# Kernel tuning notes

Measured on AMD Instinct MI355X. Metric: run time of the kernel, lower is better.

The kernel has to match this reference:

```python
import jax, jax.numpy as jnp
import numpy as np
import math

RES = 320
DECIMATION = 4
M = RES * RES // DECIMATION  # 25600 trajectory points
OVERSAMP = 1.25
WIDTH = 4
BETA = math.pi * (((WIDTH / OVERSAMP) * (OVERSAMP - 0.5)) ** 2 - 0.8) ** 0.5
B = 16


def setup_inputs() -> dict:
    key = jax.random.key(0)
    k1, k2 = jax.random.split(key)
    k_space_input = jax.random.normal(k1, (B, 1, RES, RES, 2), dtype=jnp.float32)
    # learnable k-space trajectory, coords in [-RES/2, RES/2)
    trajectory = (jax.random.uniform(k2, (M, 2), dtype=jnp.float32) - 0.5) * RES
    return {"k_space_input": k_space_input, "trajectory": trajectory}


def _grid_sample_bilinear(img, traj):
    # img: [B, C, H, W]; traj: [M, 2] = (x, y) in [-res/2, res/2]
    # Matches torch grid_sample(align_corners=True, padding_mode='zeros')
    # after normalizing traj by (res/2).
    Bn, C, H, W = img.shape
    gx = traj[:, 0] / (W / 2)
    gy = traj[:, 1] / (H / 2)
    px = (gx + 1.0) * 0.5 * (W - 1)
    py = (gy + 1.0) * 0.5 * (H - 1)
    x0 = jnp.floor(px)
    y0 = jnp.floor(py)
    wx1 = px - x0
    wy1 = py - y0
    out = jnp.zeros((Bn, C, traj.shape[0]), img.dtype)
    for dy in (0, 1):
        for dx in (0, 1):
            xi = x0 + dx
            yi = y0 + dy
            w = (wx1 if dx else 1.0 - wx1) * (wy1 if dy else 1.0 - wy1)
            inb = (xi >= 0) & (xi < W) & (yi >= 0) & (yi < H)
            xc = jnp.clip(xi, 0, W - 1).astype(jnp.int32)
            yc = jnp.clip(yi, 0, H - 1).astype(jnp.int32)
            out = out + img[:, :, yc, xc] * (w * inb)[None, None, :]
    return out  # [B, C, M]


def _kb_weight(delta, half):
    # Kaiser-Bessel interpolation kernel (sigpy convention, 1/width factor per dim)
    x = delta / half
    t = jnp.maximum(1.0 - x * x, 0.0)
    return jnp.i0(BETA * jnp.sqrt(t)) / WIDTH


def _nufft_adjoint(y, coord, H, W):
    # y: [B, M] complex64; coord: [M,2], coord[:,0]->H axis, coord[:,1]->W axis
    osH = math.ceil(OVERSAMP * H)
    osW = math.ceil(OVERSAMP * W)
    scale = jnp.array([osH / H, osW / W], jnp.float32)
    shift = jnp.array([osH // 2, osW // 2], jnp.float32)
    c = coord * scale + shift  # scaled to oversampled-grid coords
    half = WIDTH / 2.0
    start = jnp.ceil(c - half)                       # [M,2]
    offs = jnp.arange(WIDTH, dtype=jnp.float32)
    idx = start[:, :, None] + offs                   # [M,2,WIDTH]
    w = _kb_weight(c[:, :, None] - idx, half)        # [M,2,WIDTH]
    iy = idx[:, 0].astype(jnp.int32) % osH           # [M,WIDTH]
    ix = idx[:, 1].astype(jnp.int32) % osW
    ww = w[:, 0, :, None] * w[:, 1, None, :]         # [M,WIDTH,WIDTH]
    flat = (iy[:, :, None] * osW + ix[:, None, :]).reshape(-1)  # [M*WIDTH^2]
    Bn = y.shape[0]
    contrib = (y[:, :, None, None] * ww[None]).reshape(Bn, -1)  # [B, M*WIDTH^2]
    grid = jnp.zeros((Bn, osH * osW), y.dtype).at[:, flat].add(contrib)
    grid = grid.reshape(Bn, osH, osW)
    # centered unnormalized-to-ortho IFFT (sigpy scaling)
    img = jnp.fft.fftshift(
        jnp.fft.ifft2(jnp.fft.ifftshift(grid, axes=(-2, -1)), axes=(-2, -1)),
        axes=(-2, -1))
    img = img * ((osH * osW) / math.sqrt(H * W))
    sy = osH // 2 - H // 2
    sx = osW // 2 - W // 2
    img = img[:, sy:sy + H, sx:sx + W]  # center crop

    def apod(n, os_n):
        a = jnp.sqrt(jnp.maximum(
            BETA ** 2 - (np.pi * WIDTH * (jnp.arange(n, dtype=jnp.float32) - n // 2) / os_n) ** 2,
            1e-12))
        return a / jnp.sinh(a)

    img = img * apod(H, osH)[:, None] * apod(W, osW)[None, :]
    return img  # [B, H, W] complex


def reference(k_space_input, trajectory):
    # [B,1,H,W,2] -> [B,2,H,W] (real/imag channels)
    ksp = jnp.transpose(k_space_input, (0, 1, 4, 2, 3))[:, 0]
    sub = _grid_sample_bilinear(ksp, trajectory)          # [B,2,M]
    y = (sub[:, 0] + 1j * sub[:, 1]).astype(jnp.complex64)
    img = _nufft_adjoint(y, trajectory, ksp.shape[-2], ksp.shape[-1])
    out = jnp.stack([img.real, img.imag], axis=1)          # [B,2,H,W]
    return out[:, None]                                    # [B,1,2,H,W]
```

## Files before the change

### kernel.cpp

```cpp
#include <hip/hip_runtime.h>
#include <hip/hip_fp16.h>

#define NPTS   25600
#define NB     16
#define NRES   320
#define OS     400
#define NCELL  (OS * OS)
#define CAP    16
#define MAXOVF 4096

#define NJA    8
#define NJB    5
#define FFTTH  512
#define LSTRV  404

#define BETA_F (3.14159265358979f * 2.22710574513201f)

struct H2X2 { __half2 a, b; };

__device__ __forceinline__ float bessel_i0f(float x) {
    float ax = fabsf(x);
    if (ax < 3.75f) {
        float t = (ax * ax) * (1.0f / 14.0625f);
        return 1.0f + t * (3.5156229f + t * (3.0899424f + t * (1.2067492f +
                     t * (0.2659732f + t * (0.0360768f + t * 0.0045813f)))));
    } else {
        float t = 3.75f / ax;
        return (expf(ax) * rsqrtf(ax)) *
               (0.39894228f + t * (0.01328592f + t * (0.00225319f + t * (-0.00157565f +
                t * (0.00916281f + t * (-0.02057706f + t * (0.02635537f +
                t * (-0.01647633f + t * 0.00392377f))))))));
    }
}

struct OvfEntry { int cell; int m; float w; float pad; };

__global__ __launch_bounds__(1024)
void k_transpose(const float2* __restrict__ ksp, float2* __restrict__ kspT,
                 int* __restrict__ cursor, int* __restrict__ ovf_cnt)
{
    __shared__ float2 T[8 * 8 * 17];
    int tid = threadIdx.x;
    int bx = blockIdx.x % 40, by = blockIdx.x / 40;
    int x0 = bx * 8, y0 = by * 8;

    int cbase = blockIdx.x * 100;
    if (tid < 100) cursor[cbase + tid] = 0;
    if (blockIdx.x == 0 && tid >= 100 && tid < 116) ovf_cnt[tid - 100] = 0;

    int b  = tid >> 6, yl = (tid >> 3) & 7, xl = tid & 7;
    T[(yl * 8 + xl) * 17 + b] = ksp[((size_t)b * NRES + (y0 + yl)) * NRES + x0 + xl];
    __syncthreads();

    int yl2 = tid >> 7, xl2 = (tid >> 4) & 7, b2 = tid & 15;
    kspT[((size_t)(y0 + yl2) * NRES + x0 + xl2) * NB + b2] = T[(yl2 * 8 + xl2) * 17 + b2];
}

__global__ __launch_bounds__(256)
void k_sample_taps(const float2* __restrict__ kspT,
                   const float* __restrict__ traj,
                   float2* __restrict__ val,
                   int* __restrict__ cursor,
                   float2* __restrict__ entries,
                   int* __restrict__ ovf_cnt,
                   OvfEntry* __restrict__ ovf)
{
    int blk = blockIdx.x;
    if (blk < 1600) {
        int gid = blk * 256 + threadIdx.x;
        int b = gid & 15;
        int m = gid >> 4;

        float tx = traj[2 * m + 0];
        float ty = traj[2 * m + 1];

        float px = (tx * (1.0f / 160.0f) + 1.0f) * 0.5f * 319.0f;
        float py = (ty * (1.0f / 160.0f) + 1.0f) * 0.5f * 319.0f;
        float fx0 = floorf(px), fy0 = floorf(py);
        int x0 = (int)fx0, y0 = (int)fy0;
        float wx1 = px - fx0, wy1 = py - fy0;
        float wx0 = 1.0f - wx1, wy0 = 1.0f - wy1;

        const float2* row0 = kspT + ((size_t)y0 * NRES + x0) * NB + b;
        const float2* row1 = row0 + (size_t)NRES * NB;
        float2 v00 = row0[0];
        float2 v01 = row0[NB];
        float2 v10 = row1[0];
        float2 v11 = row1[NB];
        float sr = (v00.x * wx0 + v01.x * wx1) * wy0 + (v10.x * wx0 + v11.x * wx1) * wy1;
        float si = (v00.y * wx0 + v01.y * wx1) * wy0 + (v10.y * wx0 + v11.y * wx1) * wy1;

        val[gid] = make_float2(sr, si);
    } else {
        int g = (blk - 1600) * 256 + threadIdx.x;
        int m = g >> 2;
        int tq = g & 3;
        if (m >= NPTS) return;

        float tx = traj[2 * m + 0];
        float ty = traj[2 * m + 1];
        float c0 = tx * 1.25f + 200.0f;
        float c1 = ty * 1.25f + 200.0f;
        float s0 = ceilf(c0 - 2.0f);
        float s1 = ceilf(c1 - 2.0f);

        float id0 = s0 + (float)tq;
        float d0 = (c0 - id0) * 0.5f;
        float t0v = fmaxf(1.0f - d0 * d0, 0.0f);
        float w0 = bessel_i0f(BETA_F * sqrtf(t0v)) * (0.25f / 320.0f);
        int   i0 = (((int)id0) + OS) % OS;

        float w1[4];
        int   i1[4];
#pragma unroll
        for (int t = 0; t < 4; t++) {
            float id1 = s1 + (float)t;
            float d1 = (c1 - id1) * 0.5f;
            float t1 = fmaxf(1.0f - d1 * d1, 0.0f);
            w1[t] = bessel_i0f(BETA_F * sqrtf(t1)) * 0.25f;
            i1[t] = (((int)id1) + OS) % OS;
        }

#pragma unroll
        for (int t1 = 0; t1 < 4; t1++) {
            int cell = i1[t1] * OS + i0;
            float w = w0 * w1[t1];
            int slot = atomicAdd(&cursor[cell], 1);
            if (slot < CAP) {
                entries[(size_t)slot * NCELL + cell] = make_float2(__int_as_float(m), w);
            } else {
                int oi = atomicAdd(ovf_cnt, 1);
                if (oi < MAXOVF) { ovf[oi].cell = cell; ovf[oi].m = m; ovf[oi].w = w; }
            }
        }
    }
}

__global__ __launch_bounds__(256)
void k_gather(const int* __restrict__ cursor,
              const float2* __restrict__ entries,
              const float4* __restrict__ val4,
              __half2* __restrict__ grid,
              const int* __restrict__ ovf_cnt,
              const OvfEntry* __restrict__ ovf)
{
    int t = threadIdx.x;
    int half = t >> 7;
    int cell = blockIdx.x * 128 + (t & 127);
    if (cell >= NCELL) return;
    int cnt_raw = cursor[cell];
    int cnt = min(cnt_raw, CAP);

    float4 acc[4];
#pragma unroll
    for (int q = 0; q < 4; q++) acc[q] = make_float4(0.f, 0.f, 0.f, 0.f);

    for (int k = 0; k < cnt; k++) {
        float2 e = entries[(size_t)k * NCELL + cell];
        int m = __float_as_int(e.x);
        float w = e.y;
        const float4* v = val4 + (size_t)m * 8 + half * 4;
#pragma unroll
        for (int q = 0; q < 4; q++) {
            float4 x = v[q];
            acc[q].x = fmaf(w, x.x, acc[q].x);
            acc[q].y = fmaf(w, x.y, acc[q].y);
            acc[q].z = fmaf(w, x.z, acc[q].z);
            acc[q].w = fmaf(w, x.w, acc[q].w);
        }
    }

    if (cnt_raw > CAP) {
        int n = min(*ovf_cnt, MAXOVF);
        for (int i = 0; i < n; i++) {
            if (ovf[i].cell != cell) continue;
            int m = ovf[i].m;
            float w = ovf[i].w;
            const float4* v = val4 + (size_t)m * 8 + half * 4;
#pragma unroll
            for (int q = 0; q < 4; q++) {
                float4 x = v[q];
                acc[q].x = fmaf(w, x.x, acc[q].x);
                acc[q].y = fmaf(w, x.y, acc[q].y);
                acc[q].z = fmaf(w, x.z, acc[q].z);
                acc[q].w = fmaf(w, x.w, acc[q].w);
            }
        }
    }

#pragma unroll
    for (int q = 0; q < 4; q++) {
        int p = half * 8 + 2 * q;
        grid[(size_t)(p + 0) * NCELL + cell] = __float22half2_rn(make_float2(acc[q].x, acc[q].y));
        grid[(size_t)(p + 1) * NCELL + cell] = __float22half2_rn(make_float2(acc[q].z, acc[q].w));
    }
}

__device__ __forceinline__ void dft20_conj(const float2* __restrict__ Al, int off, int kh,
                                           const float2* __restrict__ E20t,
                                           float& y1r, float& y1i, float& y2r, float& y2i)
{
    float2 x0 = Al[off], x10 = Al[off + 200];
    if (kh == 0) {
        float br = x0.x + x10.x, bi = x0.y + x10.y;
        float ar = 0.f, ai = 0.f, dr = 0.f, di = 0.f;
#pragma unroll
        for (int j = 1; j <= 9; j++) {
            float2 xa = Al[off + 20 * j];
            float2 xb = Al[off + 400 - 20 * j];
            float pr = xa.x + xb.x, pi = xa.y + xb.y;
            ar += pr; ai += pi;
            float sg = (j & 1) ? -1.f : 1.f;
            dr = fmaf(sg, pr, dr); di = fmaf(sg, pi, di);
        }
        y1r = br + ar; y1i = bi + ai;
        y2r = br + dr; y2i = bi + di;
    } else {
        float sgn = (kh & 1) ? -1.f : 1.f;
        float br = fmaf(sgn, x10.x, x0.x), bi = fmaf(sgn, x10.y, x0.y);
        float2 ek = E20t[kh];
        float c = ek.x, s = ek.y;
        float Asr = 0.f, Asi = 0.f, Bsr = 0.f, Bsi = 0.f;
#pragma unroll
        for (int j = 1; j <= 9; j++) {
            float2 xa = Al[off + 20 * j];
            float2 xb = Al[off + 400 - 20 * j];
            float pr = xa.x + xb.x, pi = xa.y + xb.y;
            float mr = xa.x - xb.x, mi = xa.y - xb.y;
            Asr = fmaf(c, pr, Asr); Asi = fmaf(c, pi, Asi);
            Bsr = fmaf(s, mi, Bsr); Bsi = fmaf(s, mr, Bsi);
            float cn = c * ek.x - s * ek.y;
            s = c * ek.y + s * ek.x;
            c = cn;
        }
        y1r = br + Asr - Bsr; y1i = bi + Asi + Bsi;
        y2r = br + Asr + Bsr; y2i = bi + Asi - Bsi;
    }
}

__device__ __forceinline__ float apodf(int i) {
    float t = (float)(i - 160) * 0.031415926535897932f;
    float a = sqrtf(fmaxf(BETA_F * BETA_F - t * t, 1e-12f));
    return a / sinhf(a);
}

__global__ __launch_bounds__(FFTTH, 4)
void k_fft_pass_a(const __half2* __restrict__ grid, __half2* __restrict__ At)
{
    __shared__ __align__(16) float2 A[NJA * LSTRV];
    __shared__ float2 E20t[20];
    __shared__ float2 E400p[424];
    int tid = threadIdx.x;
    int b = blockIdx.y;
    int j0 = blockIdx.x * NJA;

    if (tid < 400) {
        float sn, cs;
        sincosf((float)tid * 0.015707963267948966f, &sn, &cs);
        E400p[tid + (tid >> 4)] = make_float2(cs, sn);
    } else if (tid >= 448 && tid < 468) {
        int t = tid - 448;
        float sn, cs;
        sincosf((float)t * 0.3141592653589793f, &sn, &cs);
        E20t[t] = make_float2(cs, sn);
    }

    const H2X2* g2 = (const H2X2*)(grid + (size_t)b * NCELL + (size_t)j0 * OS);
    for (int o = tid; o < NJA * 200; o += FFTTH) {
        int r = o / 200, q = o - r * 200;
        H2X2 v = g2[o];
        A[r * LSTRV + 2 * q]     = __half22float2(v.a);
        A[r * LSTRV + 2 * q + 1] = __half22float2(v.b);
    }
    __syncthreads();

    float v1r[4], v1i[4], v2r[4], v2i[4];
#pragma unroll
    for (int it = 0; it < 4; it++) {
        int o = tid + it * FFTTH;
        if (o < NJA * 200) {
            int r = o / 200, q = o - r * 200;
            int kh = q / 20, n2 = q - kh * 20;
            float y1r, y1i, y2r, y2i;
            dft20_conj(&A[r * LSTRV], n2, kh, E20t, y1r, y1i, y2r, y2i);
            if (kh == 0) {
                v1r[it] = y1r; v1i[it] = y1i;
                int ti = 10 * n2;
                float2 tw = E400p[ti + (ti >> 4)];
                v2r[it] = y2r * tw.x - y2i * tw.y; v2i[it] = y2r * tw.y + y2i * tw.x;
            } else {
                int t1 = n2 * kh, t2 = n2 * (20 - kh);
                float2 w1 = E400p[t1 + (t1 >> 4)], w2 = E400p[t2 + (t2 >> 4)];
                v1r[it] = y1r * w1.x - y1i * w1.y; v1i[it] = y1r * w1.y + y1i * w1.x;
                v2r[it] = y2r * w2.x - y2i * w2.y; v2i[it] = y2r * w2.y + y2i * w2.x;
            }
        }
    }
    __syncthreads();
#pragma unroll
    for (int it = 0; it < 4; it++) {
        int o = tid + it * FFTTH;
        if (o < NJA * 200) {
            int r = o / 200, q = o - r * 200;
            int kh = q / 20, n2 = q - kh * 20;
            float2* Al = &A[r * LSTRV + 20 * n2];
            if (kh == 0) {
                Al[0]  = make_float2(v1r[it], v1i[it]);
                Al[10] = make_float2(v2r[it], v2i[it]);
            } else {
                Al[kh]      = make_float2(v1r[it], v1i[it]);
                Al[20 - kh] = make_float2(v2r[it], v2i[it]);
            }
        }
    }
    __syncthreads();

#pragma unroll
    for (int it = 0; it < 3; it++) {
        int o = tid + it * FFTTH;
        if (o < NJA * 180) {
            int r = o / 180, q = o - r * 180;
            int k2h = q / 20, k1 = q - k2h * 20;
            float y1r, y1i, y2r, y2i;
            dft20_conj(&A[r * LSTRV], k1, k2h, E20t, y1r, y1i, y2r, y2i);
            v1r[it] = y1r; v1i[it] = y1i;
            v2r[it] = y2r; v2i[it] = y2i;
        }
    }
    __syncthreads();
#pragma unroll
    for (int it = 0; it < 3; it++) {
        int o = tid + it * FFTTH;
        if (o < NJA * 180) {
            int r = o / 180, q = o - r * 180;
            int k2h = q / 20, k1 = q - k2h * 20;
            float2* Al = &A[r * LSTRV];
            if (k2h == 0) {
                Al[k1] = make_float2(v1r[it], v1i[it]);
            } else {
                if (k2h <= 7)
                    Al[20 * k2h + k1] = make_float2(v1r[it], v1i[it]);
                Al[320 - 20 * k2h + k1] = make_float2(v2r[it], v2i[it]);
            }
        }
    }
    __syncthreads();

    for (int o = tid; o < 320 * NJA; o += FFTTH) {
        int uc = o >> 3, r = o & 7;
        At[((size_t)b * 320 + uc) * OS + j0 + r] = __float22half2_rn(A[r * LSTRV + uc]);
    }
}

__global__ __launch_bounds__(FFTTH, 4)
void k_fft_pass_b(const __half2* __restrict__ At, float* __restrict__ out)
{
    __shared__ __align__(16) float2 A[NJB * LSTRV];
    __shared__ float2 E20t[20];
    __shared__ float2 E400p[424];
    __shared__ float apodT[320];
    int tid = threadIdx.x;
    int b = blockIdx.y;
    int uc0 = blockIdx.x * NJB;

    if (tid < 400) {
        float sn, cs;
        sincosf((float)tid * 0.015707963267948966f, &sn, &cs);
        E400p[tid + (tid >> 4)] = make_float2(cs, sn);
    } else if (tid >= 448 && tid < 468) {
        int t = tid - 448;
        float sn, cs;
        sincosf((float)t * 0.3141592653589793f, &sn, &cs);
        E20t[t] = make_float2(cs, sn);
    }
    if (tid < 320) apodT[tid] = apodf(tid);

    const H2X2* a2 = (const H2X2*)(At + ((size_t)b * 320 + uc0) * OS);
    for (int o = tid; o < NJB * 200; o += FFTTH) {
        int r = o / 200, q = o - r * 200;
        H2X2 v = a2[o];
        A[r * LSTRV + 2 * q]     = __half22float2(v.a);
        A[r * LSTRV + 2 * q + 1] = __half22float2(v.b);
    }
    __syncthreads();

    float v1r[2], v1i[2], v2r[2], v2i[2];
#pragma unroll
    for (int it = 0; it < 2; it++) {
        int o = tid + it * FFTTH;
        if (o < NJB * 200) {
            int r = o / 200, q = o - r * 200;
            int kh = q / 20, n2 = q - kh * 20;
            float y1r, y1i, y2r, y2i;
            dft20_conj(&A[r * LSTRV], n2, kh, E20t, y1r, y1i, y2r, y2i);
            if (kh == 0) {
                v1r[it] = y1r; v1i[it] = y1i;
                int ti = 10 * n2;
                float2 tw = E400p[ti + (ti >> 4)];
                v2r[it] = y2r * tw.x - y2i * tw.y; v2i[it] = y2r * tw.y + y2i * tw.x;
            } else {
                int t1 = n2 * kh, t2 = n2 * (20 - kh);
                float2 w1 = E400p[t1 + (t1 >> 4)], w2 = E400p[t2 + (t2 >> 4)];
                v1r[it] = y1r * w1.x - y1i * w1.y; v1i[it] = y1r * w1.y + y1i * w1.x;
                v2r[it] = y2r * w2.x - y2i * w2.y; v2i[it] = y2r * w2.y + y2i * w2.x;
            }
        }
    }
    __syncthreads();
#pragma unroll
    for (int it = 0; it < 2; it++) {
        int o = tid + it * FFTTH;
        if (o < NJB * 200) {
            int r = o / 200, q = o - r * 200;
            int kh = q / 20, n2 = q - kh * 20;
            float2* Al = &A[r * LSTRV + 20 * n2];
            if (kh == 0) {
                Al[0]  = make_float2(v1r[it], v1i[it]);
                Al[10] = make_float2(v2r[it], v2i[it]);
            } else {
                Al[kh]      = make_float2(v1r[it], v1i[it]);
                Al[20 - kh] = make_float2(v2r[it], v2i[it]);
            }
        }
    }
    __syncthreads();

    for (int o = tid; o < NJB * 180; o += FFTTH) {
        int r = o / 180, q = o - r * 180;
        int k2h = q / 20, k1 = q - k2h * 20;
        float y1r, y1i, y2r, y2i;
        dft20_conj(&A[r * LSTRV], k1, k2h, E20t, y1r, y1i, y2r, y2i);

        int y = uc0 + r + 160; if (y >= 320) y -= 320;
        float apy = apodT[y];
        float* o0 = out + (((size_t)b * 2 + 0) * NRES + y) * NRES;
        float* o1 = out + (((size_t)b * 2 + 1) * NRES + y) * NRES;

        if (k2h <= 7) {
            int vc = 20 * k2h + k1;
            int x = vc + 160; if (x >= 320) x -= 320;
            float sg = ((x + y) & 1) ? -1.0f : 1.0f;
            float sc = sg * apy * apodT[x];
            o0[x] = y1r * sc;
            o1[x] = y1i * sc;
        }
        if (k2h >= 1) {
            int vc = 320 - 20 * k2h + k1;
            int x = vc + 160; if (x >= 320) x -= 320;
            float sg = ((x + y) & 1) ? -1.0f : 1.0f;
            float sc = sg * apy * apodT[x];
            o0[x] = y2r * sc;
            o1[x] = y2i * sc;
        }
    }
}

extern "C" void kernel_launch(void* const* d_in, const int* in_sizes, int n_in,
                              void* d_out, int out_size, void* d_ws, size_t ws_size,
                              hipStream_t stream) {
    const float* ksp  = (const float*)d_in[0];
    const float* traj = (const float*)d_in[1];
    float* out = (float*)d_out;

    float* base = (float*)d_ws;
    __half2* grid_h = (__half2*)base;
    __half2* At_h   = (__half2*)(base + (size_t)NB * NCELL);
    float2* entries = (float2*)(base + (size_t)NB * NCELL + (size_t)NB * 320 * OS);
    float2* val  = entries + (size_t)CAP * NCELL;
    float2* kspT = val + (size_t)NPTS * NB;
    int* cursor  = (int*)(kspT + (size_t)NRES * NRES * NB);
    int* ovf_cnt = cursor + NCELL;
    OvfEntry* ovf = (OvfEntry*)(ovf_cnt + 16);

    k_transpose  <<<dim3(1600), 1024, 0, stream>>>((const float2*)ksp, kspT, cursor, ovf_cnt);
    k_sample_taps<<<dim3(2000), 256, 0, stream>>>(kspT, traj, val, cursor, entries, ovf_cnt, ovf);
    k_gather     <<<dim3(NCELL / 128), 256, 0, stream>>>(cursor, entries, (const float4*)val,
                                                         grid_h, ovf_cnt, ovf);
    k_fft_pass_a <<<dim3(OS / NJA, NB),  FFTTH, 0, stream>>>(grid_h, At_h);
    k_fft_pass_b <<<dim3(320 / NJB, NB), FFTTH, 0, stream>>>(At_h, out);
}
```

Measured before the change: 131.0 us.

## Fuse cell gather into first FFT pass and spread taps over threads

Removes the separate gather kernel and the half-precision oversampled grid buffer. The first FFT pass now builds each row in shared memory directly from the per-cell entry lists and the sampled values, accumulating in fp32. This saves one launch plus a full grid write and read-back. The tap-binning kernel also moves from 4 threads per point to 16, one thread per 2D tap, to expose more parallelism. In exchange, every batch block re-reads the cell entry lists and does scattered 8-byte value loads, which is 16x redundant index traffic compared with the old gather that served all batches at once.

Measured after the change: 173.3 us. 1.32x slower.

```diff
diff --git a/kernel.cpp b/kernel.cpp
--- a/kernel.cpp
+++ b/kernel.cpp
@@ -93,106 +93,38 @@
         val[gid] = make_float2(sr, si);
     } else {
         int g = (blk - 1600) * 256 + threadIdx.x;
-        int m = g >> 2;
-        int tq = g & 3;
-        if (m >= NPTS) return;
+        int m   = g >> 4;
+        int tap = g & 15;
+        int t0  = tap & 3, t1 = tap >> 2;
 
         float tx = traj[2 * m + 0];
         float ty = traj[2 * m + 1];
         float c0 = tx * 1.25f + 200.0f;
         float c1 = ty * 1.25f + 200.0f;
-        float s0 = ceilf(c0 - 2.0f);
-        float s1 = ceilf(c1 - 2.0f);
-
-        float id0 = s0 + (float)tq;
+        float s0f = ceilf(c0 - 2.0f);
+        float s1f = ceilf(c1 - 2.0f);
+
+        float id0 = s0f + (float)t0;
         float d0 = (c0 - id0) * 0.5f;
         float t0v = fmaxf(1.0f - d0 * d0, 0.0f);
         float w0 = bessel_i0f(BETA_F * sqrtf(t0v)) * (0.25f / 320.0f);
         int   i0 = (((int)id0) + OS) % OS;
 
-        float w1[4];
-        int   i1[4];
-#pragma unroll
-        for (int t = 0; t < 4; t++) {
-            float id1 = s1 + (float)t;
-            float d1 = (c1 - id1) * 0.5f;
-            float t1 = fmaxf(1.0f - d1 * d1, 0.0f);
-            w1[t] = bessel_i0f(BETA_F * sqrtf(t1)) * 0.25f;
-            i1[t] = (((int)id1) + OS) % OS;
-        }
-
-#pragma unroll
-        for (int t1 = 0; t1 < 4; t1++) {
-            int cell = i1[t1] * OS + i0;
-            float w = w0 * w1[t1];
-            int slot = atomicAdd(&cursor[cell], 1);
-            if (slot < CAP) {
-                entries[(size_t)slot * NCELL + cell] = make_float2(__int_as_float(m), w);
-            } else {
-                int oi = atomicAdd(ovf_cnt, 1);
-                if (oi < MAXOVF) { ovf[oi].cell = cell; ovf[oi].m = m; ovf[oi].w = w; }
-            }
-        }
-    }
-}
-
-__global__ __launch_bounds__(256)
-void k_gather(const int* __restrict__ cursor,
-              const float2* __restrict__ entries,
-              const float4* __restrict__ val4,
-              __half2* __restrict__ grid,
-              const int* __restrict__ ovf_cnt,
-              const OvfEntry* __restrict__ ovf)
-{
-    int t = threadIdx.x;
-    int half = t >> 7;
-    int cell = blockIdx.x * 128 + (t & 127);
-    if (cell >= NCELL) return;
-    int cnt_raw = cursor[cell];
-    int cnt = min(cnt_raw, CAP);
-
-    float4 acc[4];
-#pragma unroll
-    for (int q = 0; q < 4; q++) acc[q] = make_float4(0.f, 0.f, 0.f, 0.f);
-
-    for (int k = 0; k < cnt; k++) {
-        float2 e = entries[(size_t)k * NCELL + cell];
-        int m = __float_as_int(e.x);
-        float w = e.y;
-        const float4* v = val4 + (size_t)m * 8 + half * 4;
-#pragma unroll
-        for (int q = 0; q < 4; q++) {
-            float4 x = v[q];
-            acc[q].x = fmaf(w, x.x, acc[q].x);
-            acc[q].y = fmaf(w, x.y, acc[q].y);
-            acc[q].z = fmaf(w, x.z, acc[q].z);
-            acc[q].w = fmaf(w, x.w, acc[q].w);
-        }
-    }
-
-    if (cnt_raw > CAP) {
-        int n = min(*ovf_cnt, MAXOVF);
-        for (int i = 0; i < n; i++) {
-            if (ovf[i].cell != cell) continue;
-            int m = ovf[i].m;
-            float w = ovf[i].w;
-            const float4* v = val4 + (size_t)m * 8 + half * 4;
-#pragma unroll
-            for (int q = 0; q < 4; q++) {
-                float4 x = v[q];
-                acc[q].x = fmaf(w, x.x, acc[q].x);
-                acc[q].y = fmaf(w, x.y, acc[q].y);
-                acc[q].z = fmaf(w, x.z, acc[q].z);
-                acc[q].w = fmaf(w, x.w, acc[q].w);
-            }
-        }
-    }
-
-#pragma unroll
-    for (int q = 0; q < 4; q++) {
-        int p = half * 8 + 2 * q;
-        grid[(size_t)(p + 0) * NCELL + cell] = __float22half2_rn(make_float2(acc[q].x, acc[q].y));
-        grid[(size_t)(p + 1) * NCELL + cell] = __float22half2_rn(make_float2(acc[q].z, acc[q].w));
+        float id1 = s1f + (float)t1;
+        float d1 = (c1 - id1) * 0.5f;
+        float t1v = fmaxf(1.0f - d1 * d1, 0.0f);
+        float w1 = bessel_i0f(BETA_F * sqrtf(t1v)) * 0.25f;
+        int   i1 = (((int)id1) + OS) % OS;
+
+        int cell = i1 * OS + i0;
+        float w = w0 * w1;
+        int slot = atomicAdd(&cursor[cell], 1);
+        if (slot < CAP) {
+            entries[(size_t)slot * NCELL + cell] = make_float2(__int_as_float(m), w);
+        } else {
+            int oi = atomicAdd(ovf_cnt, 1);
+            if (oi < MAXOVF) { ovf[oi].cell = cell; ovf[oi].m = m; ovf[oi].w = w; }
+        }
     }
 }
 
@@ -245,7 +177,12 @@
 }
 
 __global__ __launch_bounds__(FFTTH, 4)
-void k_fft_pass_a(const __half2* __restrict__ grid, __half2* __restrict__ At)
+void k_fft_pass_a(const int* __restrict__ cursor,
+                  const float2* __restrict__ entries,
+                  const float2* __restrict__ val,
+                  const int* __restrict__ ovf_cnt,
+                  const OvfEntry* __restrict__ ovf,
+                  __half2* __restrict__ At)
 {
     __shared__ __align__(16) float2 A[NJA * LSTRV];
     __shared__ float2 E20t[20];
@@ -265,12 +202,30 @@
         E20t[t] = make_float2(cs, sn);
     }
 
-    const H2X2* g2 = (const H2X2*)(grid + (size_t)b * NCELL + (size_t)j0 * OS);
-    for (int o = tid; o < NJA * 200; o += FFTTH) {
-        int r = o / 200, q = o - r * 200;
-        H2X2 v = g2[o];
-        A[r * LSTRV + 2 * q]     = __half22float2(v.a);
-        A[r * LSTRV + 2 * q + 1] = __half22float2(v.b);
+    for (int o = tid; o < NJA * OS; o += FFTTH) {
+        int r = o / OS, x = o - r * OS;
+        int cell = (j0 + r) * OS + x;
+        int cnt_raw = cursor[cell];
+        int cnt = min(cnt_raw, CAP);
+        float ar = 0.f, ai = 0.f;
+        for (int k = 0; k < cnt; k++) {
+            float2 e = entries[(size_t)k * NCELL + cell];
+            int mm = __float_as_int(e.x);
+            float w = e.y;
+            float2 v = val[(size_t)mm * NB + b];
+            ar = fmaf(w, v.x, ar);
+            ai = fmaf(w, v.y, ai);
+        }
+        if (cnt_raw > CAP) {
+            int n = min(*ovf_cnt, MAXOVF);
+            for (int i = 0; i < n; i++) {
+                if (ovf[i].cell != cell) continue;
+                float2 v = val[(size_t)ovf[i].m * NB + b];
+                ar = fmaf(ovf[i].w, v.x, ar);
+                ai = fmaf(ovf[i].w, v.y, ai);
+            }
+        }
+        A[r * LSTRV + x] = make_float2(ar, ai);
     }
     __syncthreads();
 
@@ -463,9 +418,8 @@
     float* out = (float*)d_out;
 
     float* base = (float*)d_ws;
-    __half2* grid_h = (__half2*)base;
-    __half2* At_h   = (__half2*)(base + (size_t)NB * NCELL);
-    float2* entries = (float2*)(base + (size_t)NB * NCELL + (size_t)NB * 320 * OS);
+    __half2* At_h   = (__half2*)base;
+    float2* entries = (float2*)(base + (size_t)NB * 320 * OS);
     float2* val  = entries + (size_t)CAP * NCELL;
     float2* kspT = val + (size_t)NPTS * NB;
     int* cursor  = (int*)(kspT + (size_t)NRES * NRES * NB);
@@ -473,9 +427,7 @@
     OvfEntry* ovf = (OvfEntry*)(ovf_cnt + 16);
 
     k_transpose  <<<dim3(1600), 1024, 0, stream>>>((const float2*)ksp, kspT, cursor, ovf_cnt);
-    k_sample_taps<<<dim3(2000), 256, 0, stream>>>(kspT, traj, val, cursor, entries, ovf_cnt, ovf);
-    k_gather     <<<dim3(NCELL / 128), 256, 0, stream>>>(cursor, entries, (const float4*)val,
-                                                         grid_h, ovf_cnt, ovf);
-    k_fft_pass_a <<<dim3(OS / NJA, NB),  FFTTH, 0, stream>>>(grid_h, At_h);
+    k_sample_taps<<<dim3(3200), 256, 0, stream>>>(kspT, traj, val, cursor, entries, ovf_cnt, ovf);
+    k_fft_pass_a <<<dim3(OS / NJA, NB),  FFTTH, 0, stream>>>(cursor, entries, val, ovf_cnt, ovf, At_h);
     k_fft_pass_b <<<dim3(320 / NJB, NB), FFTTH, 0, stream>>>(At_h, out);
 }
```

## Fuse sampling, tap binning and gather into one cooperative kernel with grid sync

Applied to the files above, without the earlier changes.

Merges the bilinear sampling/tap-binning kernel and the per-cell gather kernel into one cooperative kernel. The two phases are separated by a grid-wide barrier and use grid-stride loops over 1024 blocks of 256 threads. Tap work is also remapped so each thread computes one of the 16 taps rather than four, which spreads the Bessel evaluations and atomics across more lanes. This removes one kernel launch boundary, but adds grid-sync cost and requires all 1024 blocks to be co-resident.

After: 238.9 us. 1.82x slower.

```diff
diff --git a/kernel.cpp b/kernel.cpp
--- a/kernel.cpp
+++ b/kernel.cpp
@@ -1,5 +1,8 @@
 #include <hip/hip_runtime.h>
 #include <hip/hip_fp16.h>
+#include <hip/hip_cooperative_groups.h>
+
+namespace cg = cooperative_groups;
 
 #define NPTS   25600
 #define NB     16
@@ -13,6 +16,10 @@
 #define NJB    5
 #define FFTTH  512
 #define LSTRV  404
+
+#define MIDBLK 1024
+#define MIDTH  256
+#define MIDN   (MIDBLK * MIDTH)
 
 #define BETA_F (3.14159265358979f * 2.22710574513201f)
 
@@ -56,75 +63,66 @@
     kspT[((size_t)(y0 + yl2) * NRES + x0 + xl2) * NB + b2] = T[(yl2 * 8 + xl2) * 17 + b2];
 }
 
-__global__ __launch_bounds__(256)
-void k_sample_taps(const float2* __restrict__ kspT,
-                   const float* __restrict__ traj,
-                   float2* __restrict__ val,
-                   int* __restrict__ cursor,
-                   float2* __restrict__ entries,
-                   int* __restrict__ ovf_cnt,
-                   OvfEntry* __restrict__ ovf)
+__global__ __launch_bounds__(MIDTH, 4)
+void k_mid(const float2* __restrict__ kspT,
+           const float* __restrict__ traj,
+           float2* __restrict__ val,
+           int* __restrict__ cursor,
+           float2* __restrict__ entries,
+           int* __restrict__ ovf_cnt,
+           OvfEntry* __restrict__ ovf,
+           __half2* __restrict__ grid)
 {
-    int blk = blockIdx.x;
-    if (blk < 1600) {
-        int gid = blk * 256 + threadIdx.x;
-        int b = gid & 15;
-        int m = gid >> 4;
-
+    cg::grid_group gg = cg::this_grid();
+    int gtid = blockIdx.x * MIDTH + threadIdx.x;
+
+    for (int i = gtid; i < NPTS * NB; i += MIDN) {
+        int m = i >> 4;
         float tx = traj[2 * m + 0];
         float ty = traj[2 * m + 1];
 
-        float px = (tx * (1.0f / 160.0f) + 1.0f) * 0.5f * 319.0f;
-        float py = (ty * (1.0f / 160.0f) + 1.0f) * 0.5f * 319.0f;
-        float fx0 = floorf(px), fy0 = floorf(py);
-        int x0 = (int)fx0, y0 = (int)fy0;
-        float wx1 = px - fx0, wy1 = py - fy0;
-        float wx0 = 1.0f - wx1, wy0 = 1.0f - wy1;
-
-        const float2* row0 = kspT + ((size_t)y0 * NRES + x0) * NB + b;
-        const float2* row1 = row0 + (size_t)NRES * NB;
-        float2 v00 = row0[0];
-        float2 v01 = row0[NB];
-        float2 v10 = row1[0];
-        float2 v11 = row1[NB];
-        float sr = (v00.x * wx0 + v01.x * wx1) * wy0 + (v10.x * wx0 + v11.x * wx1) * wy1;
-        float si = (v00.y * wx0 + v01.y * wx1) * wy0 + (v10.y * wx0 + v11.y * wx1) * wy1;
-
-        val[gid] = make_float2(sr, si);
-    } else {
-        int g = (blk - 1600) * 256 + threadIdx.x;
-        int m = g >> 2;
-        int tq = g & 3;
-        if (m >= NPTS) return;
-
-        float tx = traj[2 * m + 0];
-        float ty = traj[2 * m + 1];
-        float c0 = tx * 1.25f + 200.0f;
-        float c1 = ty * 1.25f + 200.0f;
-        float s0 = ceilf(c0 - 2.0f);
-        float s1 = ceilf(c1 - 2.0f);
-
-        float id0 = s0 + (float)tq;
-        float d0 = (c0 - id0) * 0.5f;
-        float t0v = fmaxf(1.0f - d0 * d0, 0.0f);
-        float w0 = bessel_i0f(BETA_F * sqrtf(t0v)) * (0.25f / 320.0f);
-        int   i0 = (((int)id0) + OS) % OS;
-
-        float w1[4];
-        int   i1[4];
-#pragma unroll
-        for (int t = 0; t < 4; t++) {
-            float id1 = s1 + (float)t;
+        {
+            int b = i & 15;
+            float px = (tx * (1.0f / 160.0f) + 1.0f) * 0.5f * 319.0f;
+            float py = (ty * (1.0f / 160.0f) + 1.0f) * 0.5f * 319.0f;
+            float fx0 = floorf(px), fy0 = floorf(py);
+            int x0 = (int)fx0, y0 = (int)fy0;
+            float wx1 = px - fx0, wy1 = py - fy0;
+            float wx0 = 1.0f - wx1, wy0 = 1.0f - wy1;
+
+            const float2* row0 = kspT + ((size_t)y0 * NRES + x0) * NB + b;
+            const float2* row1 = row0 + (size_t)NRES * NB;
+            float2 v00 = row0[0];
+            float2 v01 = row0[NB];
+            float2 v10 = row1[0];
+            float2 v11 = row1[NB];
+            float sr = (v00.x * wx0 + v01.x * wx1) * wy0 + (v10.x * wx0 + v11.x * wx1) * wy1;
+            float si = (v00.y * wx0 + v01.y * wx1) * wy0 + (v10.y * wx0 + v11.y * wx1) * wy1;
+            val[i] = make_float2(sr, si);
+        }
+
+        {
+            int tap = i & 15;
+            int t0 = tap & 3, t1 = tap >> 2;
+            float c0 = tx * 1.25f + 200.0f;
+            float c1 = ty * 1.25f + 200.0f;
+            float s0f = ceilf(c0 - 2.0f);
+            float s1f = ceilf(c1 - 2.0f);
+
+            float id0 = s0f + (float)t0;
+            float d0 = (c0 - id0) * 0.5f;
+            float t0v = fmaxf(1.0f - d0 * d0, 0.0f);
+            float w0 = bessel_i0f(BETA_F * sqrtf(t0v)) * (0.25f / 320.0f);
+            int   i0 = (((int)id0) + OS) % OS;
+
+            float id1 = s1f + (float)t1;
             float d1 = (c1 - id1) * 0.5f;
-            float t1 = fmaxf(1.0f - d1 * d1, 0.0f);
-            w1[t] = bessel_i0f(BETA_F * sqrtf(t1)) * 0.25f;
-            i1[t] = (((int)id1) + OS) % OS;
-        }
-
-#pragma unroll
-        for (int t1 = 0; t1 < 4; t1++) {
-            int cell = i1[t1] * OS + i0;
-            float w = w0 * w1[t1];
+            float t1v = fmaxf(1.0f - d1 * d1, 0.0f);
+            float w1 = bessel_i0f(BETA_F * sqrtf(t1v)) * 0.25f;
+            int   i1 = (((int)id1) + OS) % OS;
+
+            int cell = i1 * OS + i0;
+            float w = w0 * w1;
             int slot = atomicAdd(&cursor[cell], 1);
             if (slot < CAP) {
                 entries[(size_t)slot * NCELL + cell] = make_float2(__int_as_float(m), w);
@@ -134,48 +132,27 @@
             }
         }
     }
-}
-
-__global__ __launch_bounds__(256)
-void k_gather(const int* __restrict__ cursor,
-              const float2* __restrict__ entries,
-              const float4* __restrict__ val4,
-              __half2* __restrict__ grid,
-              const int* __restrict__ ovf_cnt,
-              const OvfEntry* __restrict__ ovf)
-{
-    int t = threadIdx.x;
-    int half = t >> 7;
-    int cell = blockIdx.x * 128 + (t & 127);
-    if (cell >= NCELL) return;
-    int cnt_raw = cursor[cell];
-    int cnt = min(cnt_raw, CAP);
-
-    float4 acc[4];
-#pragma unroll
-    for (int q = 0; q < 4; q++) acc[q] = make_float4(0.f, 0.f, 0.f, 0.f);
-
-    for (int k = 0; k < cnt; k++) {
-        float2 e = entries[(size_t)k * NCELL + cell];
-        int m = __float_as_int(e.x);
-        float w = e.y;
-        const float4* v = val4 + (size_t)m * 8 + half * 4;
-#pragma unroll
-        for (int q = 0; q < 4; q++) {
-            float4 x = v[q];
-            acc[q].x = fmaf(w, x.x, acc[q].x);
-            acc[q].y = fmaf(w, x.y, acc[q].y);
-            acc[q].z = fmaf(w, x.z, acc[q].z);
-            acc[q].w = fmaf(w, x.w, acc[q].w);
-        }
-    }
-
-    if (cnt_raw > CAP) {
-        int n = min(*ovf_cnt, MAXOVF);
-        for (int i = 0; i < n; i++) {
-            if (ovf[i].cell != cell) continue;
-            int m = ovf[i].m;
-            float w = ovf[i].w;
+
+    gg.sync();
+
+    const float4* val4 = (const float4*)val;
+    for (int i = gtid; i < NCELL * 2; i += MIDN) {
+        int t = i & 255;
+        int vb = i >> 8;
+        int half = t >> 7;
+        int cell = vb * 128 + (t & 127);
+
+        int cnt_raw = cursor[cell];
+        int cnt = min(cnt_raw, CAP);
+
+        float4 acc[4];
+#pragma unroll
+        for (int q = 0; q < 4; q++) acc[q] = make_float4(0.f, 0.f, 0.f, 0.f);
+
+        for (int k = 0; k < cnt; k++) {
+            float2 e = entries[(size_t)k * NCELL + cell];
+            int m = __float_as_int(e.x);
+            float w = e.y;
             const float4* v = val4 + (size_t)m * 8 + half * 4;
 #pragma unroll
             for (int q = 0; q < 4; q++) {
@@ -186,13 +163,31 @@
                 acc[q].w = fmaf(w, x.w, acc[q].w);
             }
         }
-    }
-
-#pragma unroll
-    for (int q = 0; q < 4; q++) {
-        int p = half * 8 + 2 * q;
-        grid[(size_t)(p + 0) * NCELL + cell] = __float22half2_rn(make_float2(acc[q].x, acc[q].y));
-        grid[(size_t)(p + 1) * NCELL + cell] = __float22half2_rn(make_float2(acc[q].z, acc[q].w));
+
+        if (cnt_raw > CAP) {
+            int n = min(*ovf_cnt, MAXOVF);
+            for (int o = 0; o < n; o++) {
+                if (ovf[o].cell != cell) continue;
+                int m = ovf[o].m;
+                float w = ovf[o].w;
+                const float4* v = val4 + (size_t)m * 8 + half * 4;
+#pragma unroll
+                for (int q = 0; q < 4; q++) {
+                    float4 x = v[q];
+                    acc[q].x = fmaf(w, x.x, acc[q].x);
+                    acc[q].y = fmaf(w, x.y, acc[q].y);
+                    acc[q].z = fmaf(w, x.z, acc[q].z);
+                    acc[q].w = fmaf(w, x.w, acc[q].w);
+                }
+            }
+        }
+
+#pragma unroll
+        for (int q = 0; q < 4; q++) {
+            int p = half * 8 + 2 * q;
+            grid[(size_t)(p + 0) * NCELL + cell] = __float22half2_rn(make_float2(acc[q].x, acc[q].y));
+            grid[(size_t)(p + 1) * NCELL + cell] = __float22half2_rn(make_float2(acc[q].z, acc[q].w));
+        }
     }
 }
 
@@ -472,10 +467,13 @@
     int* ovf_cnt = cursor + NCELL;
     OvfEntry* ovf = (OvfEntry*)(ovf_cnt + 16);
 
-    k_transpose  <<<dim3(1600), 1024, 0, stream>>>((const float2*)ksp, kspT, cursor, ovf_cnt);
-    k_sample_taps<<<dim3(2000), 256, 0, stream>>>(kspT, traj, val, cursor, entries, ovf_cnt, ovf);
-    k_gather     <<<dim3(NCELL / 128), 256, 0, stream>>>(cursor, entries, (const float4*)val,
-                                                         grid_h, ovf_cnt, ovf);
-    k_fft_pass_a <<<dim3(OS / NJA, NB),  FFTTH, 0, stream>>>(grid_h, At_h);
-    k_fft_pass_b <<<dim3(320 / NJB, NB), FFTTH, 0, stream>>>(At_h, out);
-}
+    k_transpose<<<dim3(1600), 1024, 0, stream>>>((const float2*)ksp, kspT, cursor, ovf_cnt);
+
+    void* args[] = { (void*)&kspT, (void*)&traj, (void*)&val, (void*)&cursor,
+                     (void*)&entries, (void*)&ovf_cnt, (void*)&ovf, (void*)&grid_h };
+    hipLaunchCooperativeKernel((const void*)k_mid, dim3(MIDBLK), dim3(MIDTH),
+                               args, 0, stream);
+
+    k_fft_pass_a<<<dim3(OS / NJA, NB),  FFTTH, 0, stream>>>(grid_h, At_h);
+    k_fft_pass_b<<<dim3(320 / NJB, NB), FFTTH, 0, stream>>>(At_h, out);
+}
```

## Store sampled values and gridding entries in half precision, one tap per thread

Applied to the files above, without the earlier changes.

Sampled k-space values are stored as half2 instead of float2, and each bin entry packs the point index and a half-precision weight into one 32-bit word. This halves the memory traffic of the gather kernel's random reads and of the entries array. The tap kernel now gives each thread one of the 16 taps rather than four, using 3200 blocks, which spreads atomics and Bessel evaluations over more threads. The cost is reduced precision in the values and weights, and the point index must fit in 16 bits (25600 does).

Result: no change. 129.9 us (median of 2 runs) (-0.8%).

```diff
diff --git a/kernel.cpp b/kernel.cpp
--- a/kernel.cpp
+++ b/kernel.cpp
@@ -59,9 +59,9 @@
 __global__ __launch_bounds__(256)
 void k_sample_taps(const float2* __restrict__ kspT,
                    const float* __restrict__ traj,
-                   float2* __restrict__ val,
+                   __half2* __restrict__ valh,
                    int* __restrict__ cursor,
-                   float2* __restrict__ entries,
+                   unsigned int* __restrict__ entries,
                    int* __restrict__ ovf_cnt,
                    OvfEntry* __restrict__ ovf)
 {
@@ -90,56 +90,50 @@
         float sr = (v00.x * wx0 + v01.x * wx1) * wy0 + (v10.x * wx0 + v11.x * wx1) * wy1;
         float si = (v00.y * wx0 + v01.y * wx1) * wy0 + (v10.y * wx0 + v11.y * wx1) * wy1;
 
-        val[gid] = make_float2(sr, si);
+        valh[gid] = __float22half2_rn(make_float2(sr, si));
     } else {
         int g = (blk - 1600) * 256 + threadIdx.x;
-        int m = g >> 2;
-        int tq = g & 3;
-        if (m >= NPTS) return;
+        int m   = g >> 4;
+        int tap = g & 15;
+        int t0  = tap & 3, t1 = tap >> 2;
 
         float tx = traj[2 * m + 0];
         float ty = traj[2 * m + 1];
         float c0 = tx * 1.25f + 200.0f;
         float c1 = ty * 1.25f + 200.0f;
-        float s0 = ceilf(c0 - 2.0f);
-        float s1 = ceilf(c1 - 2.0f);
-
-        float id0 = s0 + (float)tq;
+        float s0f = ceilf(c0 - 2.0f);
+        float s1f = ceilf(c1 - 2.0f);
+
+        float id0 = s0f + (float)t0;
         float d0 = (c0 - id0) * 0.5f;
         float t0v = fmaxf(1.0f - d0 * d0, 0.0f);
         float w0 = bessel_i0f(BETA_F * sqrtf(t0v)) * (0.25f / 320.0f);
         int   i0 = (((int)id0) + OS) % OS;
 
-        float w1[4];
-        int   i1[4];
-#pragma unroll
-        for (int t = 0; t < 4; t++) {
-            float id1 = s1 + (float)t;
-            float d1 = (c1 - id1) * 0.5f;
-            float t1 = fmaxf(1.0f - d1 * d1, 0.0f);
-            w1[t] = bessel_i0f(BETA_F * sqrtf(t1)) * 0.25f;
-            i1[t] = (((int)id1) + OS) % OS;
-        }
-
-#pragma unroll
-        for (int t1 = 0; t1 < 4; t1++) {
-            int cell = i1[t1] * OS + i0;
-            float w = w0 * w1[t1];
-            int slot = atomicAdd(&cursor[cell], 1);
-            if (slot < CAP) {
-                entries[(size_t)slot * NCELL + cell] = make_float2(__int_as_float(m), w);
-            } else {
-                int oi = atomicAdd(ovf_cnt, 1);
-                if (oi < MAXOVF) { ovf[oi].cell = cell; ovf[oi].m = m; ovf[oi].w = w; }
-            }
+        float id1 = s1f + (float)t1;
+        float d1 = (c1 - id1) * 0.5f;
+        float t1v = fmaxf(1.0f - d1 * d1, 0.0f);
+        float w1 = bessel_i0f(BETA_F * sqrtf(t1v)) * 0.25f;
+        int   i1 = (((int)id1) + OS) % OS;
+
+        int cell = i1 * OS + i0;
+        float w = w0 * w1;
+        int slot = atomicAdd(&cursor[cell], 1);
+        if (slot < CAP) {
+            unsigned int pk = ((unsigned int)m << 16) |
+                              (unsigned int)__half_as_ushort(__float2half(w));
+            entries[(size_t)slot * NCELL + cell] = pk;
+        } else {
+            int oi = atomicAdd(ovf_cnt, 1);
+            if (oi < MAXOVF) { ovf[oi].cell = cell; ovf[oi].m = m; ovf[oi].w = w; }
         }
     }
 }
 
 __global__ __launch_bounds__(256)
 void k_gather(const int* __restrict__ cursor,
-              const float2* __restrict__ entries,
-              const float4* __restrict__ val4,
+              const unsigned int* __restrict__ entries,
+              const uint4* __restrict__ valq,
               __half2* __restrict__ grid,
               const int* __restrict__ ovf_cnt,
               const OvfEntry* __restrict__ ovf)
@@ -147,26 +141,33 @@
     int t = threadIdx.x;
     int half = t >> 7;
     int cell = blockIdx.x * 128 + (t & 127);
-    if (cell >= NCELL) return;
     int cnt_raw = cursor[cell];
     int cnt = min(cnt_raw, CAP);
 
-    float4 acc[4];
-#pragma unroll
-    for (int q = 0; q < 4; q++) acc[q] = make_float4(0.f, 0.f, 0.f, 0.f);
+    float2 acc[8];
+#pragma unroll
+    for (int q = 0; q < 8; q++) acc[q] = make_float2(0.f, 0.f);
 
     for (int k = 0; k < cnt; k++) {
-        float2 e = entries[(size_t)k * NCELL + cell];
-        int m = __float_as_int(e.x);
-        float w = e.y;
-        const float4* v = val4 + (size_t)m * 8 + half * 4;
+        unsigned int e = entries[(size_t)k * NCELL + cell];
+        int m = (int)(e >> 16);
+        float w = __half2float(__ushort_as_half((unsigned short)(e & 0xFFFFu)));
+        const uint4* v = valq + (size_t)m * 4 + half * 2;
+        uint4 u0 = v[0];
+        uint4 u1 = v[1];
+        const __half2* h0 = (const __half2*)&u0;
+        const __half2* h1 = (const __half2*)&u1;
 #pragma unroll
         for (int q = 0; q < 4; q++) {
-            float4 x = v[q];
+            float2 x = __half22float2(h0[q]);
             acc[q].x = fmaf(w, x.x, acc[q].x);
             acc[q].y = fmaf(w, x.y, acc[q].y);
-            acc[q].z = fmaf(w, x.z, acc[q].z);
-            acc[q].w = fmaf(w, x.w, acc[q].w);
+        }
+#pragma unroll
+        for (int q = 0; q < 4; q++) {
+            float2 x = __half22float2(h1[q]);
+            acc[4 + q].x = fmaf(w, x.x, acc[4 + q].x);
+            acc[4 + q].y = fmaf(w, x.y, acc[4 + q].y);
         }
     }
 
@@ -176,23 +177,30 @@
             if (ovf[i].cell != cell) continue;
             int m = ovf[i].m;
             float w = ovf[i].w;
-            const float4* v = val4 + (size_t)m * 8 + half * 4;
+            const uint4* v = valq + (size_t)m * 4 + half * 2;
+            uint4 u0 = v[0];
+            uint4 u1 = v[1];
+            const __half2* h0 = (const __half2*)&u0;
+            const __half2* h1 = (const __half2*)&u1;
 #pragma unroll
             for (int q = 0; q < 4; q++) {
-                float4 x = v[q];
+                float2 x = __half22float2(h0[q]);
                 acc[q].x = fmaf(w, x.x, acc[q].x);
                 acc[q].y = fmaf(w, x.y, acc[q].y);
-                acc[q].z = fmaf(w, x.z, acc[q].z);
-                acc[q].w = fmaf(w, x.w, acc[q].w);
-            }
-        }
-    }
-
-#pragma unroll
-    for (int q = 0; q < 4; q++) {
-        int p = half * 8 + 2 * q;
-        grid[(size_t)(p + 0) * NCELL + cell] = __float22half2_rn(make_float2(acc[q].x, acc[q].y));
-        grid[(size_t)(p + 1) * NCELL + cell] = __float22half2_rn(make_float2(acc[q].z, acc[q].w));
+            }
+#pragma unroll
+            for (int q = 0; q < 4; q++) {
+                float2 x = __half22float2(h1[q]);
+                acc[4 + q].x = fmaf(w, x.x, acc[4 + q].x);
+                acc[4 + q].y = fmaf(w, x.y, acc[4 + q].y);
+            }
+        }
+    }
+
+#pragma unroll
+    for (int q = 0; q < 8; q++) {
+        int p = half * 8 + q;
+        grid[(size_t)p * NCELL + cell] = __float22half2_rn(acc[q]);
     }
 }
 
@@ -465,16 +473,16 @@
     float* base = (float*)d_ws;
     __half2* grid_h = (__half2*)base;
     __half2* At_h   = (__half2*)(base + (size_t)NB * NCELL);
-    float2* entries = (float2*)(base + (size_t)NB * NCELL + (size_t)NB * 320 * OS);
-    float2* val  = entries + (size_t)CAP * NCELL;
-    float2* kspT = val + (size_t)NPTS * NB;
-    int* cursor  = (int*)(kspT + (size_t)NRES * NRES * NB);
-    int* ovf_cnt = cursor + NCELL;
+    unsigned int* entries = (unsigned int*)(base + (size_t)NB * NCELL + (size_t)NB * 320 * OS);
+    __half2* valh = (__half2*)(entries + (size_t)CAP * NCELL);
+    float2* kspT  = (float2*)(valh + (size_t)NPTS * NB);
+    int* cursor   = (int*)(kspT + (size_t)NRES * NRES * NB);
+    int* ovf_cnt  = cursor + NCELL;
     OvfEntry* ovf = (OvfEntry*)(ovf_cnt + 16);
 
     k_transpose  <<<dim3(1600), 1024, 0, stream>>>((const float2*)ksp, kspT, cursor, ovf_cnt);
-    k_sample_taps<<<dim3(2000), 256, 0, stream>>>(kspT, traj, val, cursor, entries, ovf_cnt, ovf);
-    k_gather     <<<dim3(NCELL / 128), 256, 0, stream>>>(cursor, entries, (const float4*)val,
+    k_sample_taps<<<dim3(3200), 256, 0, stream>>>(kspT, traj, valh, cursor, entries, ovf_cnt, ovf);
+    k_gather     <<<dim3(NCELL / 128), 256, 0, stream>>>(cursor, entries, (const uint4*)valh,
                                                          grid_h, ovf_cnt, ovf);
     k_fft_pass_a <<<dim3(OS / NJA, NB),  FFTTH, 0, stream>>>(grid_h, At_h);
     k_fft_pass_b <<<dim3(320 / NJB, NB), FFTTH, 0, stream>>>(At_h, out);
```
